# Optimization experiments

Hardware: AMD Instinct MI355X
Metric: run time of the kernel (lower is better)

Reference implementation:

```python
import jax, jax.numpy as jnp
import numpy as np

B, S, D, H, L, V, FFM = 4, 2048, 512, 8, 6, 8000, 4
HD = D // H
FF = FFM * D


def setup_inputs() -> dict:
    key = jax.random.key(0)
    ks = jax.random.split(key, 12)
    sc = 0.02
    return {
        "tokens": jax.random.randint(ks[0], (B, S), 0, V),
        "embed": jax.random.normal(ks[1], (V, D), jnp.float32) * sc,
        "wq": jax.random.normal(ks[2], (L, D, D), jnp.float32) * sc,
        "wk": jax.random.normal(ks[3], (L, D, D), jnp.float32) * sc,
        "wv": jax.random.normal(ks[4], (L, D, D), jnp.float32) * sc,
        "wo": jax.random.normal(ks[5], (L, D, D), jnp.float32) * sc,
        "bo": jnp.zeros((L, D), jnp.float32),
        "w1": jax.random.normal(ks[6], (L, D, FF), jnp.float32) * sc,
        "b1": jnp.zeros((L, FF), jnp.float32),
        "w2": jax.random.normal(ks[7], (L, FF, D), jnp.float32) * sc,
        "b2": jnp.zeros((L, D), jnp.float32),
        "ln_g": jnp.ones((L, D), jnp.float32),
        "ln_b": jnp.zeros((L, D), jnp.float32),
        "lnf_g": jnp.ones((D,), jnp.float32),
        "lnf_b": jnp.zeros((D,), jnp.float32),
        "w_out": jax.random.normal(ks[8], (D, V), jnp.float32) * sc,
        "b_out": jnp.zeros((V,), jnp.float32),
    }


def _layernorm(x, g, b, eps=1e-5):
    m = jnp.mean(x, -1, keepdims=True)
    v = jnp.var(x, -1, keepdims=True)
    return (x - m) * jax.lax.rsqrt(v + eps) * g + b


def _pos_encoding():
    pos = jnp.arange(S, dtype=jnp.float32)[:, None]
    div = jnp.exp(jnp.arange(0, D, 2, dtype=jnp.float32) * (-np.log(10000.0) / D))
    pe = jnp.zeros((S, D), jnp.float32)
    pe = pe.at[:, 0::2].set(jnp.sin(pos * div))
    pe = pe.at[:, 1::2].set(jnp.cos(pos * div))
    return pe


def _forward(tokens, embed, wq, wk, wv, wo, bo, w1, b1, w2, b2, ln_g, ln_b,
             lnf_g, lnf_b, w_out, b_out):
    x = embed[tokens] + _pos_encoding()[None]  # [B,S,D]
    causal = jnp.tril(jnp.ones((S, S), bool))
    neg_inf = jnp.float32(-jnp.inf)
    # NOTE: original scales scores by 1/sqrt(n_embd) (key.weight.size(-1) == D)
    inv_scale = 1.0 / jnp.sqrt(jnp.float32(D))

    def block(x, p):
        pwq, pwk, pwv, pwo, pbo, pw1, pb1, pw2, pb2, g, b = p
        # attention sublayer (same LayerNorm params used for both sublayers,
        # matching the repo's reuse of add_and_norm_1)
        h = _layernorm(x, g, b)
        q = (h @ pwq).reshape(B, S, H, HD)
        k = (h @ pwk).reshape(B, S, H, HD)
        v = (h @ pwv).reshape(B, S, H, HD)
        scores = jnp.einsum('bqhd,bkhd->bhqk', q, k) * inv_scale
        scores = jnp.where(causal, scores, neg_inf)
        att = jax.nn.softmax(scores, axis=-1)
        o = jnp.einsum('bhqk,bkhd->bqhd', att, v).reshape(B, S, D)
        x = x + o @ pwo + pbo
        # FFN sublayer
        h2 = _layernorm(x, g, b)
        x = x + jax.nn.relu(h2 @ pw1 + pb1) @ pw2 + pb2
        return x, None

    params = (wq, wk, wv, wo, bo, w1, b1, w2, b2, ln_g, ln_b)
    x, _ = jax.lax.scan(block, x, params)
    x = _layernorm(x, lnf_g, lnf_b)
    logits = x @ w_out + b_out  # [B,S,V]
    return logits


def reference(tokens, embed, wq, wk, wv, wo, bo, w1, b1, w2, b2, ln_g, ln_b,
              lnf_g, lnf_b, w_out, b_out):
    return _forward(tokens, embed, wq, wk, wv, wo, bo, w1, b1, w2, b2,
                    ln_g, ln_b, lnf_g, lnf_b, w_out, b_out)
```

## Files before the change

### kernel.cpp

```cpp
#include <hip/hip_runtime.h>
#include <hip/hip_bf16.h>

#define Bsz 4
#define Ssz 2048
#define Dsz 512
#define Hsz 8
#define Lsz 6
#define Vsz 8000
#define FFsz 2048
#define Msz (Bsz*Ssz)
#define VszPad 8192

typedef unsigned short u16;
typedef unsigned int u32;
typedef __attribute__((ext_vector_type(8))) short bf16x8;
typedef __attribute__((ext_vector_type(4))) float f32x4;
typedef __attribute__((ext_vector_type(16))) float f32x16;
typedef __attribute__((ext_vector_type(4))) u32 u32x4;
typedef __attribute__((ext_vector_type(4))) u16 u16x4;

__device__ __forceinline__ u16 f2b(float f) {
    union { float f; unsigned u; } x; x.f = f;
    return (u16)((x.u + 0x7fffu + ((x.u >> 16) & 1u)) >> 16);
}
__device__ __forceinline__ u16 f2bn(float f) {
    __hip_bfloat16 h = __float2bfloat16(f);
    return __builtin_bit_cast(u16, h);
}
__device__ __forceinline__ float b2f(u16 v) {
    union { u32 u; float f; } x; x.u = ((u32)v) << 16; return x.f;
}

#define GLOAD_LDS16(g, l) __builtin_amdgcn_global_load_lds( \
    (const __attribute__((address_space(1))) u32*)(g), \
    (__attribute__((address_space(3))) u32*)(l), 16, 0, 0)

__global__ __launch_bounds__(256) void embed_kernel(const int* __restrict__ tokens,
                                                    const float* __restrict__ embed,
                                                    u16* __restrict__ x) {
    int idx = blockIdx.x * 256 + threadIdx.x;
    int row = idx >> 8, p = idx & 255;
    int tok = tokens[row];
    int s = row & (Ssz - 1);
    float div = __expf((float)p * (-9.210340371976184f / 256.f));
    float ang = (float)s * div;
    float2 e = ((const float2*)(embed + (size_t)tok * Dsz))[p];
    u32 o = (u32)f2b(e.x + sinf(ang)) | ((u32)f2b(e.y + cosf(ang)) << 16);
    ((u32*)(x + (size_t)row * Dsz))[p] = o;
}

__global__ __launch_bounds__(256) void ln_kernel(const u16* __restrict__ x,
                                                 const float* __restrict__ g,
                                                 const float* __restrict__ bta,
                                                 u16* __restrict__ out) {
    int wave = threadIdx.x >> 6, lane = threadIdx.x & 63;
    int row = blockIdx.x * 4 + wave;
    bf16x8 a = ((const bf16x8*)(x + (size_t)row * Dsz))[lane];
    float vals[8];
    #pragma unroll
    for (int i = 0; i < 8; ++i) vals[i] = b2f((u16)a[i]);
    float s = 0.f;
    #pragma unroll
    for (int i = 0; i < 8; ++i) s += vals[i];
    #pragma unroll
    for (int o = 32; o; o >>= 1) s += __shfl_xor(s, o);
    float mean = s * (1.f / 512.f);
    float sq = 0.f;
    #pragma unroll
    for (int i = 0; i < 8; ++i) { float d = vals[i] - mean; sq += d * d; }
    #pragma unroll
    for (int o = 32; o; o >>= 1) sq += __shfl_xor(sq, o);
    float rstd = rsqrtf(sq * (1.f / 512.f) + 1e-5f);
    int base = lane * 8;
    bf16x8 rv;
    #pragma unroll
    for (int i = 0; i < 8; ++i)
        rv[i] = (short)f2b((vals[i] - mean) * rstd * g[base + i] + bta[base + i]);
    *(bf16x8*)(out + (size_t)row * Dsz + base) = rv;
}

__global__ __launch_bounds__(256) void tconv_kernel(const float* __restrict__ src,
                                                    u16* __restrict__ dst,
                                                    int R, int C,
                                                    size_t sstride, size_t dstride) {
    __shared__ float tile[32][33];
    const float* s = src + blockIdx.z * sstride;
    u16* d = dst + blockIdx.z * dstride;
    int c0 = blockIdx.x * 32, r0 = blockIdx.y * 32;
    int tx = threadIdx.x & 31, ty = threadIdx.x >> 5;
    #pragma unroll
    for (int i = 0; i < 32; i += 8)
        tile[ty + i][tx] = s[(size_t)(r0 + ty + i) * C + c0 + tx];
    __syncthreads();
    #pragma unroll
    for (int i = 0; i < 32; i += 8)
        d[(size_t)(c0 + ty + i) * R + r0 + tx] = f2b(tile[tx][ty + i]);
}

__global__ __launch_bounds__(256) void tconvqkv_kernel(const float* __restrict__ wq,
                                                       const float* __restrict__ wk,
                                                       const float* __restrict__ wv,
                                                       u16* __restrict__ dst) {
    __shared__ float tile[32][33];
    int z = blockIdx.z, which = z / Lsz, l = z % Lsz;
    const float* s = (which == 0 ? wq : which == 1 ? wk : wv) + (size_t)l * Dsz * Dsz;
    u16* d = dst + ((size_t)l * 3 + which) * Dsz * Dsz;
    int c0 = blockIdx.x * 32, r0 = blockIdx.y * 32;
    int tx = threadIdx.x & 31, ty = threadIdx.x >> 5;
    #pragma unroll
    for (int i = 0; i < 32; i += 8)
        tile[ty + i][tx] = s[(size_t)(r0 + ty + i) * Dsz + c0 + tx];
    __syncthreads();
    #pragma unroll
    for (int i = 0; i < 32; i += 8)
        d[(size_t)(c0 + ty + i) * Dsz + r0 + tx] = f2b(tile[tx][ty + i]);
}

template<bool BIAS, bool RES, bool RELU, bool OF32, bool OBF16, bool XN, int BMF, bool QKV>
__global__ __launch_bounds__(256, 4) void gemm_kernel(const u16* __restrict__ A,
                                                   const u16* __restrict__ BT,
                                                   const float* __restrict__ bias,
                                                   const u16* __restrict__ res,
                                                   float* __restrict__ outf,
                                                   u16* __restrict__ outb,
                                                   u16* __restrict__ vT,
                                                   int M, int N, int K) {
    __shared__ u16 As[BMF * 32 * 64];
    __shared__ u16 Bs[128 * 64];
    int tid = threadIdx.x;
    int wave = tid >> 6, lane = tid & 63;
    int wm = wave >> 1, wn = wave & 1;
    int gx = gridDim.x;
    int bid = blockIdx.y * gx + blockIdx.x;
    int xcd = bid & 7, j = bid >> 3;
    int mblk, nblk;
    if (XN) { mblk = j >> 3; nblk = xcd * 8 + (j & 7); }
    else    { int sm = gridDim.y >> 3; mblk = xcd * sm + j / gx; nblk = j % gx; }
    int m0 = mblk * (BMF * 32), n0 = nblk * 128;
    int lr = lane & 15, lg = lane >> 4;
    int srow = lane >> 3;
    int scol = (lane & 7) * 8;
    f32x4 acc[BMF][4] = {};
    for (int k0 = 0; k0 < K; k0 += 64) {
        #pragma unroll
        for (int i = 0; i < BMF; ++i) {
            int chunk = wave * BMF + i;
            int r = chunk * 8 + srow;
            GLOAD_LDS16(A + (size_t)(m0 + r) * K + k0 + scol, &As[chunk * 512]);
        }
        #pragma unroll
        for (int i = 0; i < 4; ++i) {
            int chunk = wave * 4 + i;
            int r = chunk * 8 + srow;
            GLOAD_LDS16(BT + (size_t)(n0 + r) * K + k0 + scol, &Bs[chunk * 512]);
        }
        __syncthreads();
        #pragma unroll
        for (int kk = 0; kk < 2; ++kk) {
            bf16x8 af[BMF], bfr[4];
            #pragma unroll
            for (int m = 0; m < BMF; ++m)
                af[m] = *(const bf16x8*)(As + (wm * (BMF * 16) + m * 16 + lr) * 64 + kk * 32 + lg * 8);
            #pragma unroll
            for (int n = 0; n < 4; ++n)
                bfr[n] = *(const bf16x8*)(Bs + (wn * 64 + n * 16 + lr) * 64 + kk * 32 + lg * 8);
            #pragma unroll
            for (int m = 0; m < BMF; ++m)
                #pragma unroll
                for (int n = 0; n < 4; ++n)
                    acc[m][n] = __builtin_amdgcn_mfma_f32_16x16x32_bf16(af[m], bfr[n], acc[m][n], 0, 0, 0);
        }
        __syncthreads();
    }
    #pragma unroll
    for (int m = 0; m < BMF; ++m) {
        int row = m0 + wm * (BMF * 16) + m * 16 + lg * 4;
        #pragma unroll
        for (int n = 0; n < 4; ++n) {
            int col = n0 + wn * 64 + n * 16 + lr;
            if (QKV && col >= 1024) {
                int hd = col - 1024;
                int hh = hd >> 6; hd &= 63;
                int b = row >> 11, s = row & 2047;
                u16x4 v4;
                #pragma unroll
                for (int j2 = 0; j2 < 4; ++j2) v4[j2] = f2b(acc[m][n][j2]);
                *(u16x4*)(vT + ((size_t)(b * 8 + hh) * 64 + hd) * Ssz + s) = v4;
            } else if (col < N) {
                float bv = BIAS ? bias[col] : 0.f;
                #pragma unroll
                for (int j2 = 0; j2 < 4; ++j2) {
                    float v = acc[m][n][j2] + bv;
                    if (RES) v += b2f(res[(size_t)(row + j2) * N + col]);
                    if (RELU) v = fmaxf(v, 0.f);
                    if (OF32) outf[(size_t)(row + j2) * N + col] = v;
                    if (OBF16) outb[(size_t)(row + j2) * N + col] = f2b(v);
                }
            }
        }
    }
}

template<bool BIAS, bool RELU, bool OF32, bool XN>
__global__ __launch_bounds__(512, 2) void gemmBig_kernel(const u16* __restrict__ A,
                                                         const u16* __restrict__ BT,
                                                         const float* __restrict__ bias,
                                                         float* __restrict__ outf,
                                                         u16* __restrict__ outb,
                                                         int M, int N, int K) {
    __shared__ u16 As[256 * 64];
    __shared__ u16 Bs[128 * 64];
    int tid = threadIdx.x;
    int wave = tid >> 6, lane = tid & 63;
    int wm = wave >> 1, wn = wave & 1;
    int gx = gridDim.x;
    int bid = blockIdx.y * gx + blockIdx.x;
    int xcd = bid & 7, j = bid >> 3;
    int mblk, nblk;
    if (XN) { mblk = j >> 3; nblk = xcd * 8 + (j & 7); }
    else    { int sm = gridDim.y >> 3; mblk = xcd * sm + j / gx; nblk = j % gx; }
    int m0 = mblk * 256, n0 = nblk * 128;
    int lr = lane & 15, lg = lane >> 4;
    int srow = lane >> 3;
    int scol = (lane & 7) * 8;
    f32x4 acc[4][4] = {};
    for (int k0 = 0; k0 < K; k0 += 64) {
        #pragma unroll
        for (int i = 0; i < 4; ++i) {
            int chunk = wave * 4 + i;
            GLOAD_LDS16(A + (size_t)(m0 + chunk * 8 + srow) * K + k0 + scol, &As[chunk * 512]);
        }
        #pragma unroll
        for (int i = 0; i < 2; ++i) {
            int chunk = wave * 2 + i;
            GLOAD_LDS16(BT + (size_t)(n0 + chunk * 8 + srow) * K + k0 + scol, &Bs[chunk * 512]);
        }
        __syncthreads();
        #pragma unroll
        for (int kk = 0; kk < 2; ++kk) {
            bf16x8 af[4], bfr[4];
            #pragma unroll
            for (int m = 0; m < 4; ++m)
                af[m] = *(const bf16x8*)(As + (wm * 64 + m * 16 + lr) * 64 + kk * 32 + lg * 8);
            #pragma unroll
            for (int n = 0; n < 4; ++n)
                bfr[n] = *(const bf16x8*)(Bs + (wn * 64 + n * 16 + lr) * 64 + kk * 32 + lg * 8);
            #pragma unroll
            for (int m = 0; m < 4; ++m)
                #pragma unroll
                for (int n = 0; n < 4; ++n)
                    acc[m][n] = __builtin_amdgcn_mfma_f32_16x16x32_bf16(af[m], bfr[n], acc[m][n], 0, 0, 0);
        }
        __syncthreads();
    }
    #pragma unroll
    for (int m = 0; m < 4; ++m) {
        int row = m0 + wm * 64 + m * 16 + lg * 4;
        #pragma unroll
        for (int n = 0; n < 4; ++n) {
            int col = n0 + wn * 64 + n * 16 + lr;
            if (col < N) {
                float bv = BIAS ? bias[col] : 0.f;
                #pragma unroll
                for (int j2 = 0; j2 < 4; ++j2) {
                    float v = acc[m][n][j2] + bv;
                    if (RELU) v = fmaxf(v, 0.f);
                    if (OF32) outf[(size_t)(row + j2) * N + col] = v;
                    else      outb[(size_t)(row + j2) * N + col] = f2b(v);
                }
            }
        }
    }
}

__global__ __launch_bounds__(256, 3) void flash5_kernel(const u16* __restrict__ qkv,
                                                        const u16* __restrict__ vT,
                                                        u16* __restrict__ o) {
    __shared__ u16 Ks[2][64 * 64];
    __shared__ u16 Vs[2][64 * 64];
    int blk = blockIdx.x;
    int bh = blk & 31;
    int c = 15 - (blk >> 5);
    int b = bh >> 3, hh = bh & 7;
    int tid = threadIdx.x, wave = tid >> 6, lane = tid & 63;
    int l31 = lane & 31, h5 = lane >> 5;
    int g = c * 4 + wave;
    int qg = g * 32 + l31;
    int ext = (g >> 1) + 1;
    int nt = 2 * c + 2;
    const float cs = 0.044194173824159216f;

    bf16x8 qf[4];
    {
        const u16* qrow = qkv + (size_t)(b * Ssz + qg) * 1536 + hh * 64;
        #pragma unroll
        for (int cb = 0; cb < 4; ++cb)
            qf[cb] = *(const bf16x8*)(qrow + cb * 16 + h5 * 8);
    }
    f32x16 Oa0 = {}, Oa1 = {};
    float m_run = -1e30f, l_run = 0.f;
    int sr = tid >> 3;
    int sc2 = (tid & 7) * 8;
    const u16* kbase = qkv + (size_t)(b * Ssz) * 1536 + 512 + hh * 64;
    const u16* vbase = vT + (size_t)bh * 64 * Ssz;
    int byteA = (sr * 128 + sc2 * 2) ^ ((sr & 7) << 4);
    int byteB = ((sr + 32) * 128 + sc2 * 2) ^ ((sr & 7) << 4);

    {
        bf16x8 kA = *(const bf16x8*)(kbase + (size_t)sr * 1536 + sc2);
        bf16x8 kB = *(const bf16x8*)(kbase + (size_t)(32 + sr) * 1536 + sc2);
        bf16x8 vA = *(const bf16x8*)(vbase + (size_t)sr * Ssz + sc2);
        bf16x8 vB = *(const bf16x8*)(vbase + (size_t)(32 + sr) * Ssz + sc2);
        *(bf16x8*)((char*)Ks[0] + byteA) = kA;
        *(bf16x8*)((char*)Ks[0] + byteB) = kB;
        *(bf16x8*)((char*)Vs[0] + byteA) = vA;
        *(bf16x8*)((char*)Vs[0] + byteB) = vB;
    }
    __syncthreads();

    for (int kt = 0; kt < nt; ++kt) {
        int cur = kt & 1;
        bool pf = (kt + 1 < nt);
        bf16x8 kA, kB, vA, vB;
        if (pf) {
            kA = *(const bf16x8*)(kbase + (size_t)((kt + 1) * 64 + sr) * 1536 + sc2);
            kB = *(const bf16x8*)(kbase + (size_t)((kt + 1) * 64 + 32 + sr) * 1536 + sc2);
            vA = *(const bf16x8*)(vbase + (size_t)sr * Ssz + (kt + 1) * 64 + sc2);
            vB = *(const bf16x8*)(vbase + (size_t)(32 + sr) * Ssz + (kt + 1) * 64 + sc2);
        }
        const u16* Kc = Ks[cur];
        const u16* Vc = Vs[cur];
        if (kt < ext) {
            bool dtile = (kt == ext - 1);
            int mts = (dtile && !(g & 1)) ? 1 : 2;
            f32x16 st[2] = {};
            __builtin_amdgcn_s_setprio(1);
            #pragma unroll
            for (int mt = 0; mt < 2; ++mt)
                if (mt < mts) {
                    int r = mt * 32 + l31;
                    #pragma unroll
                    for (int cb = 0; cb < 4; ++cb) {
                        int byte = (r * 128 + (cb * 16 + h5 * 8) * 2) ^ ((r & 7) << 4);
                        bf16x8 kf = *(const bf16x8*)((char*)Kc + byte);
                        st[mt] = __builtin_amdgcn_mfma_f32_32x32x16_bf16(kf, qf[cb], st[mt], 0, 0, 0);
                    }
                }
            __builtin_amdgcn_s_setprio(0);
            float pmax = -1e30f;
            #pragma unroll
            for (int mt = 0; mt < 2; ++mt)
                if (mt < mts)
                    #pragma unroll
                    for (int r = 0; r < 16; ++r) {
                        float v = st[mt][r];
                        if (dtile) {
                            int kglob = kt * 64 + mt * 32 + (r & 3) + 8 * (r >> 2) + 4 * h5;
                            if (kglob > qg) v = -1e30f;
                        }
                        st[mt][r] = v;
                        pmax = fmaxf(pmax, v);
                    }
            pmax = fmaxf(pmax, __shfl_xor(pmax, 32));
            if (!__all(pmax - m_run <= 181.019336f)) {
                float mn = fmaxf(m_run, pmax);
                float al = __expf((m_run - mn) * cs);
                l_run *= al;
                #pragma unroll
                for (int r = 0; r < 16; ++r) {
                    int qloc = (r & 3) + 8 * (r >> 2) + 4 * h5;
                    float alr = __shfl(al, qloc);
                    Oa0[r] *= alr; Oa1[r] *= alr;
                }
                m_run = mn;
            }
            float ls = 0.f;
            u32 pk[2][8];
            #pragma unroll
            for (int mt = 0; mt < 2; ++mt)
                if (mt < mts)
                    #pragma unroll
                    for (int w = 0; w < 8; ++w) {
                        float p0 = __expf((st[mt][2 * w]     - m_run) * cs);
                        float p1 = __expf((st[mt][2 * w + 1] - m_run) * cs);
                        ls += p0 + p1;
                        pk[mt][w] = (u32)f2bn(p0) | ((u32)f2bn(p1) << 16);
                    }
            l_run += ls + __shfl_xor(ls, 32);
            __builtin_amdgcn_s_setprio(1);
            #pragma unroll
            for (int mt = 0; mt < 2; ++mt)
                if (mt < mts) {
                    u32 pko[8];
                    #pragma unroll
                    for (int w = 0; w < 8; ++w)
                        pko[w] = __shfl_xor(pk[mt][w], 32);
                    #pragma unroll
                    for (int kbl = 0; kbl < 2; ++kbl) {
                        int kb = mt * 2 + kbl;
                        u32x4 aw;
                        #pragma unroll
                        for (int w = 0; w < 4; ++w) {
                            int widx = 4 * kbl + 2 * h5 + (w & 1);
                            bool own = (w < 2) != (h5 == 1);
                            aw[w] = own ? pk[mt][widx] : pko[widx];
                        }
                        bf16x8 af = __builtin_bit_cast(bf16x8, aw);
                        #pragma unroll
                        for (int dt = 0; dt < 2; ++dt) {
                            int r = dt * 32 + l31;
                            int byte = (r * 128 + (kb * 16 + h5 * 8) * 2) ^ ((r & 7) << 4);
                            bf16x8 vf = *(const bf16x8*)((char*)Vc + byte);
                            if (dt == 0) Oa0 = __builtin_amdgcn_mfma_f32_32x32x16_bf16(af, vf, Oa0, 0, 0, 0);
                            else         Oa1 = __builtin_amdgcn_mfma_f32_32x32x16_bf16(af, vf, Oa1, 0, 0, 0);
                        }
                    }
                }
            __builtin_amdgcn_s_setprio(0);
        }
        if (pf) {
            u16* Kn = Ks[cur ^ 1];
            u16* Vn = Vs[cur ^ 1];
            *(bf16x8*)((char*)Kn + byteA) = kA;
            *(bf16x8*)((char*)Kn + byteB) = kB;
            *(bf16x8*)((char*)Vn + byteA) = vA;
            *(bf16x8*)((char*)Vn + byteB) = vB;
        }
        __syncthreads();
    }
    float rln = 1.f / l_run;
    u16* obase = o + (size_t)(b * Ssz) * Dsz + hh * 64;
    #pragma unroll
    for (int r = 0; r < 16; ++r) {
        int qloc = (r & 3) + 8 * (r >> 2) + 4 * h5;
        float s = __shfl(rln, qloc);
        u16* orow = obase + (size_t)(g * 32 + qloc) * Dsz + l31;
        orow[0]  = f2bn(Oa0[r] * s);
        orow[32] = f2bn(Oa1[r] * s);
    }
}

extern "C" void kernel_launch(void* const* d_in, const int* in_sizes, int n_in,
                              void* d_out, int out_size, void* d_ws, size_t ws_size,
                              hipStream_t stream) {
    (void)in_sizes; (void)n_in; (void)out_size; (void)ws_size;
    const int*   tokens = (const int*)d_in[0];
    const float* embed  = (const float*)d_in[1];
    const float* wq     = (const float*)d_in[2];
    const float* wk     = (const float*)d_in[3];
    const float* wv     = (const float*)d_in[4];
    const float* wo     = (const float*)d_in[5];
    const float* bo     = (const float*)d_in[6];
    const float* w1     = (const float*)d_in[7];
    const float* b1     = (const float*)d_in[8];
    const float* w2     = (const float*)d_in[9];
    const float* b2     = (const float*)d_in[10];
    const float* ln_g   = (const float*)d_in[11];
    const float* ln_b   = (const float*)d_in[12];
    const float* lnf_g  = (const float*)d_in[13];
    const float* lnf_b  = (const float*)d_in[14];
    const float* w_out  = (const float*)d_in[15];
    const float* b_out  = (const float*)d_in[16];
    float* out = (float*)d_out;

    char* ws = (char*)d_ws;
    size_t off = 0;
    auto alloc = [&](size_t bytes) {
        void* p = ws + off;
        off += (bytes + 255) & ~(size_t)255;
        return p;
    };
    u16*   x     = (u16*)alloc((size_t)Msz * Dsz * 2);
    u16*   h     = (u16*)alloc((size_t)Msz * Dsz * 2);
    u16*   qkv   = (u16*)alloc((size_t)Msz * 1536 * 2);
    u16*   vT    = (u16*)alloc((size_t)Bsz * Hsz * 64 * Ssz * 2);
    u16*   ob    = (u16*)alloc((size_t)Msz * Dsz * 2);
    u16*   ffh   = (u16*)alloc((size_t)Msz * FFsz * 2);
    u16*   wqkvT = (u16*)alloc((size_t)Lsz * 3 * Dsz * Dsz * 2);
    u16*   woT   = (u16*)alloc((size_t)Lsz * Dsz * Dsz * 2);
    u16*   w1T   = (u16*)alloc((size_t)Lsz * FFsz * Dsz * 2);
    u16*   w2T   = (u16*)alloc((size_t)Lsz * Dsz * FFsz * 2);
    u16*   w_outT= (u16*)alloc((size_t)VszPad * Dsz * 2);

    dim3 tb(256);
    size_t dd = (size_t)Dsz * Dsz;
    hipMemsetAsync(w_outT + (size_t)Vsz * Dsz, 0, (size_t)(VszPad - Vsz) * Dsz * 2, stream);
    tconvqkv_kernel<<<dim3(16, 16, Lsz * 3), tb, 0, stream>>>(wq, wk, wv, wqkvT);
    tconv_kernel<<<dim3(16, 16, Lsz), tb, 0, stream>>>(wo, woT, Dsz, Dsz, dd, dd);
    tconv_kernel<<<dim3(64, 16, Lsz), tb, 0, stream>>>(w1, w1T, Dsz, FFsz, (size_t)Dsz * FFsz, (size_t)FFsz * Dsz);
    tconv_kernel<<<dim3(16, 64, Lsz), tb, 0, stream>>>(w2, w2T, FFsz, Dsz, (size_t)FFsz * Dsz, (size_t)Dsz * FFsz);
    tconv_kernel<<<dim3(250, 16, 1), tb, 0, stream>>>(w_out, w_outT, Dsz, Vsz, 0, 0);

    embed_kernel<<<Msz * 256 / 256, tb, 0, stream>>>(tokens, embed, x);

    for (int l = 0; l < Lsz; ++l) {
        ln_kernel<<<Msz / 4, tb, 0, stream>>>(x, ln_g + l * Dsz, ln_b + l * Dsz, h);
        gemm_kernel<false, false, false, false, true, false, 4, true><<<dim3(12, Msz / 128), tb, 0, stream>>>(
            h, wqkvT + (size_t)l * 3 * dd, nullptr, nullptr, nullptr, qkv, vT, Msz, 1536, Dsz);
        flash5_kernel<<<dim3(512), tb, 0, stream>>>(qkv, vT, ob);
        gemm_kernel<true, true, false, false, true, false, 2, false><<<dim3(4, Msz / 64), tb, 0, stream>>>(
            ob, woT + (size_t)l * dd, bo + l * Dsz, x, nullptr, x, nullptr, Msz, Dsz, Dsz);
        ln_kernel<<<Msz / 4, tb, 0, stream>>>(x, ln_g + l * Dsz, ln_b + l * Dsz, h);
        gemmBig_kernel<true, true, false, false><<<dim3(16, Msz / 256), dim3(512), 0, stream>>>(
            h, w1T + (size_t)l * FFsz * Dsz, b1 + l * FFsz, nullptr, ffh, Msz, FFsz, Dsz);
        gemm_kernel<true, true, false, false, true, false, 2, false><<<dim3(4, Msz / 64), tb, 0, stream>>>(
            ffh, w2T + (size_t)l * Dsz * FFsz, b2 + l * Dsz, x, nullptr, x, nullptr, Msz, Dsz, FFsz);
    }
    ln_kernel<<<Msz / 4, tb, 0, stream>>>(x, lnf_g, lnf_b, h);
    gemmBig_kernel<true, false, true, true><<<dim3(64, Msz / 256), dim3(512), 0, stream>>>(
        h, w_outT, b_out, out, nullptr, Msz, Vsz, Dsz);
}
```

Baseline: 1.548 ms.

## Add triple-buffered swizzled-LDS GEMM and use it for QKV, FFN1 and logits

Replaces gemmBig and the QKV path of gemm_kernel with a new 512-thread gemmP kernel. It triple-buffers LDS tiles, issuing global-to-LDS loads two k-steps ahead and waiting with vmcnt counters instead of full __syncthreads, so memory latency overlaps with MFMA work. It also XOR-swizzles the LDS layout to cut bank conflicts. Triple buffering needs 144KB of LDS, which limits occupancy to one block per CU, and flash5's launch bound is relaxed to 2 blocks.

After: 1.657 ms. +7.0%, slower.

```diff
diff --git a/kernel.cpp b/kernel.cpp
--- a/kernel.cpp
+++ b/kernel.cpp
@@ -178,6 +178,102 @@
         #pragma unroll
         for (int n = 0; n < 4; ++n) {
             int col = n0 + wn * 64 + n * 16 + lr;
+            if (col < N) {
+                float bv = BIAS ? bias[col] : 0.f;
+                #pragma unroll
+                for (int j2 = 0; j2 < 4; ++j2) {
+                    float v = acc[m][n][j2] + bv;
+                    if (RES) v += b2f(res[(size_t)(row + j2) * N + col]);
+                    if (RELU) v = fmaxf(v, 0.f);
+                    if (OF32) outf[(size_t)(row + j2) * N + col] = v;
+                    if (OBF16) outb[(size_t)(row + j2) * N + col] = f2b(v);
+                }
+            }
+        }
+    }
+}
+
+template<bool BIAS, bool RELU, bool OF32, bool OBF16, bool XN, bool QKV>
+__global__ __launch_bounds__(512, 1) void gemmP_kernel(const u16* __restrict__ A,
+                                                       const u16* __restrict__ BT,
+                                                       const float* __restrict__ bias,
+                                                       float* __restrict__ outf,
+                                                       u16* __restrict__ outb,
+                                                       u16* __restrict__ vT,
+                                                       int M, int N, int K) {
+    __shared__ u16 As[3][256 * 64];
+    __shared__ u16 Bs[3][128 * 64];
+    int tid = threadIdx.x;
+    int wave = tid >> 6, lane = tid & 63;
+    int wm = wave >> 1, wn = wave & 1;
+    int gx = gridDim.x;
+    int bid = blockIdx.y * gx + blockIdx.x;
+    int xcd = bid & 7, j = bid >> 3;
+    int mblk, nblk;
+    if (XN) { int npx = gx >> 3; nblk = xcd * npx + (j % npx); mblk = j / npx; }
+    else    { int sm = gridDim.y >> 3; mblk = xcd * sm + j / gx; nblk = j % gx; }
+    int m0 = mblk * 256, n0 = nblk * 128;
+    int lr = lane & 15, lg = lane >> 4;
+    int sr8 = lane >> 3;
+    int gc16 = ((lane & 7) ^ sr8) * 8;
+    int nt = K >> 6;
+
+    auto issue = [&](int t) {
+        int rg = t % 3;
+        int k0 = t << 6;
+        #pragma unroll
+        for (int i = 0; i < 4; ++i)
+            GLOAD_LDS16(A + (size_t)(m0 + i * 64 + wave * 8 + sr8) * K + k0 + gc16,
+                        &As[rg][i * 4096 + wave * 512]);
+        #pragma unroll
+        for (int i = 0; i < 2; ++i)
+            GLOAD_LDS16(BT + (size_t)(n0 + i * 64 + wave * 8 + sr8) * K + k0 + gc16,
+                        &Bs[rg][i * 4096 + wave * 512]);
+    };
+
+    f32x4 acc[4][4] = {};
+    issue(0); issue(1);
+    __builtin_amdgcn_sched_barrier(0);
+    asm volatile("s_waitcnt vmcnt(6)\n\ts_barrier" ::: "memory");
+    __builtin_amdgcn_sched_barrier(0);
+
+    for (int t = 0; t < nt; ++t) {
+        if (t + 2 < nt) issue(t + 2);
+        const u16* Ar = As[t % 3];
+        const u16* Br = Bs[t % 3];
+        #pragma unroll
+        for (int kk = 0; kk < 2; ++kk) {
+            bf16x8 af[4], bfr[4];
+            #pragma unroll
+            for (int m = 0; m < 4; ++m) {
+                int r = wm * 64 + m * 16 + lr;
+                int slot = (kk * 4 + lg) ^ (lr & 7);
+                af[m] = *(const bf16x8*)((const char*)Ar + r * 128 + slot * 16);
+            }
+            #pragma unroll
+            for (int n = 0; n < 4; ++n) {
+                int r = wn * 64 + n * 16 + lr;
+                int slot = (kk * 4 + lg) ^ (lr & 7);
+                bfr[n] = *(const bf16x8*)((const char*)Br + r * 128 + slot * 16);
+            }
+            #pragma unroll
+            for (int m = 0; m < 4; ++m)
+                #pragma unroll
+                for (int n = 0; n < 4; ++n)
+                    acc[m][n] = __builtin_amdgcn_mfma_f32_16x16x32_bf16(af[m], bfr[n], acc[m][n], 0, 0, 0);
+        }
+        __builtin_amdgcn_sched_barrier(0);
+        if (t + 2 < nt) asm volatile("s_waitcnt vmcnt(6)\n\ts_barrier" ::: "memory");
+        else            asm volatile("s_waitcnt vmcnt(0)\n\ts_barrier" ::: "memory");
+        __builtin_amdgcn_sched_barrier(0);
+    }
+
+    #pragma unroll
+    for (int m = 0; m < 4; ++m) {
+        int row = m0 + wm * 64 + m * 16 + lg * 4;
+        #pragma unroll
+        for (int n = 0; n < 4; ++n) {
+            int col = n0 + wn * 64 + n * 16 + lr;
             if (QKV && col >= 1024) {
                 int hd = col - 1024;
                 int hh = hd >> 6; hd &= 63;
@@ -191,7 +287,6 @@
                 #pragma unroll
                 for (int j2 = 0; j2 < 4; ++j2) {
                     float v = acc[m][n][j2] + bv;
-                    if (RES) v += b2f(res[(size_t)(row + j2) * N + col]);
                     if (RELU) v = fmaxf(v, 0.f);
                     if (OF32) outf[(size_t)(row + j2) * N + col] = v;
                     if (OBF16) outb[(size_t)(row + j2) * N + col] = f2b(v);
@@ -201,79 +296,7 @@
     }
 }
 
-template<bool BIAS, bool RELU, bool OF32, bool XN>
-__global__ __launch_bounds__(512, 2) void gemmBig_kernel(const u16* __restrict__ A,
-                                                         const u16* __restrict__ BT,
-                                                         const float* __restrict__ bias,
-                                                         float* __restrict__ outf,
-                                                         u16* __restrict__ outb,
-                                                         int M, int N, int K) {
-    __shared__ u16 As[256 * 64];
-    __shared__ u16 Bs[128 * 64];
-    int tid = threadIdx.x;
-    int wave = tid >> 6, lane = tid & 63;
-    int wm = wave >> 1, wn = wave & 1;
-    int gx = gridDim.x;
-    int bid = blockIdx.y * gx + blockIdx.x;
-    int xcd = bid & 7, j = bid >> 3;
-    int mblk, nblk;
-    if (XN) { mblk = j >> 3; nblk = xcd * 8 + (j & 7); }
-    else    { int sm = gridDim.y >> 3; mblk = xcd * sm + j / gx; nblk = j % gx; }
-    int m0 = mblk * 256, n0 = nblk * 128;
-    int lr = lane & 15, lg = lane >> 4;
-    int srow = lane >> 3;
-    int scol = (lane & 7) * 8;
-    f32x4 acc[4][4] = {};
-    for (int k0 = 0; k0 < K; k0 += 64) {
-        #pragma unroll
-        for (int i = 0; i < 4; ++i) {
-            int chunk = wave * 4 + i;
-            GLOAD_LDS16(A + (size_t)(m0 + chunk * 8 + srow) * K + k0 + scol, &As[chunk * 512]);
-        }
-        #pragma unroll
-        for (int i = 0; i < 2; ++i) {
-            int chunk = wave * 2 + i;
-            GLOAD_LDS16(BT + (size_t)(n0 + chunk * 8 + srow) * K + k0 + scol, &Bs[chunk * 512]);
-        }
-        __syncthreads();
-        #pragma unroll
-        for (int kk = 0; kk < 2; ++kk) {
-            bf16x8 af[4], bfr[4];
-            #pragma unroll
-            for (int m = 0; m < 4; ++m)
-                af[m] = *(const bf16x8*)(As + (wm * 64 + m * 16 + lr) * 64 + kk * 32 + lg * 8);
-            #pragma unroll
-            for (int n = 0; n < 4; ++n)
-                bfr[n] = *(const bf16x8*)(Bs + (wn * 64 + n * 16 + lr) * 64 + kk * 32 + lg * 8);
-            #pragma unroll
-            for (int m = 0; m < 4; ++m)
-                #pragma unroll
-                for (int n = 0; n < 4; ++n)
-                    acc[m][n] = __builtin_amdgcn_mfma_f32_16x16x32_bf16(af[m], bfr[n], acc[m][n], 0, 0, 0);
-        }
-        __syncthreads();
-    }
-    #pragma unroll
-    for (int m = 0; m < 4; ++m) {
-        int row = m0 + wm * 64 + m * 16 + lg * 4;
-        #pragma unroll
-        for (int n = 0; n < 4; ++n) {
-            int col = n0 + wn * 64 + n * 16 + lr;
-            if (col < N) {
-                float bv = BIAS ? bias[col] : 0.f;
-                #pragma unroll
-                for (int j2 = 0; j2 < 4; ++j2) {
-                    float v = acc[m][n][j2] + bv;
-                    if (RELU) v = fmaxf(v, 0.f);
-                    if (OF32) outf[(size_t)(row + j2) * N + col] = v;
-                    else      outb[(size_t)(row + j2) * N + col] = f2b(v);
-                }
-            }
-        }
-    }
-}
-
-__global__ __launch_bounds__(256, 3) void flash5_kernel(const u16* __restrict__ qkv,
+__global__ __launch_bounds__(256, 2) void flash5_kernel(const u16* __restrict__ qkv,
                                                         const u16* __restrict__ vT,
                                                         u16* __restrict__ o) {
     __shared__ u16 Ks[2][64 * 64];
@@ -495,18 +518,18 @@
 
     for (int l = 0; l < Lsz; ++l) {
         ln_kernel<<<Msz / 4, tb, 0, stream>>>(x, ln_g + l * Dsz, ln_b + l * Dsz, h);
-        gemm_kernel<false, false, false, false, true, false, 4, true><<<dim3(12, Msz / 128), tb, 0, stream>>>(
-            h, wqkvT + (size_t)l * 3 * dd, nullptr, nullptr, nullptr, qkv, vT, Msz, 1536, Dsz);
+        gemmP_kernel<false, false, false, true, false, true><<<dim3(12, Msz / 256), dim3(512), 0, stream>>>(
+            h, wqkvT + (size_t)l * 3 * dd, nullptr, nullptr, qkv, vT, Msz, 1536, Dsz);
         flash5_kernel<<<dim3(512), tb, 0, stream>>>(qkv, vT, ob);
         gemm_kernel<true, true, false, false, true, false, 2, false><<<dim3(4, Msz / 64), tb, 0, stream>>>(
             ob, woT + (size_t)l * dd, bo + l * Dsz, x, nullptr, x, nullptr, Msz, Dsz, Dsz);
         ln_kernel<<<Msz / 4, tb, 0, stream>>>(x, ln_g + l * Dsz, ln_b + l * Dsz, h);
-        gemmBig_kernel<true, true, false, false><<<dim3(16, Msz / 256), dim3(512), 0, stream>>>(
-            h, w1T + (size_t)l * FFsz * Dsz, b1 + l * FFsz, nullptr, ffh, Msz, FFsz, Dsz);
+        gemmP_kernel<true, true, false, true, false, false><<<dim3(16, Msz / 256), dim3(512), 0, stream>>>(
+            h, w1T + (size_t)l * FFsz * Dsz, b1 + l * FFsz, nullptr, ffh, nullptr, Msz, FFsz, Dsz);
         gemm_kernel<true, true, false, false, true, false, 2, false><<<dim3(4, Msz / 64), tb, 0, stream>>>(
             ffh, w2T + (size_t)l * Dsz * FFsz, b2 + l * Dsz, x, nullptr, x, nullptr, Msz, Dsz, FFsz);
     }
     ln_kernel<<<Msz / 4, tb, 0, stream>>>(x, lnf_g, lnf_b, h);
-    gemmBig_kernel<true, false, true, true><<<dim3(64, Msz / 256), dim3(512), 0, stream>>>(
-        h, w_outT, b_out, out, nullptr, Msz, Vsz, Dsz);
-}
+    gemmP_kernel<true, false, true, false, true, false><<<dim3(VszPad / 128, Msz / 256), dim3(512), 0, stream>>>(
+        h, w_outT, b_out, out, nullptr, nullptr, Msz, Vsz, Dsz);
+}
```
